# Optimization experiments

Hardware: AMD Instinct MI355X
Metric: run time of the kernel (lower is better)

The kernel has to match this reference:

```python
import jax, jax.numpy as jnp
import numpy as np

D_MODEL = 1024
N_HEADS = 16
HEAD_DIM = D_MODEL // N_HEADS
THETA = 10000.0
NEG = -1e9


def apply_rope(x, positions, theta=THETA):
    # x: (B, H, S, d), positions: (B, 1, S)
    d = x.shape[-1]
    inv_freq = 1.0 / (theta ** (jnp.arange(0, d, 2, dtype=jnp.float32) / d))  # (d/2,)
    freqs = positions[..., None].astype(jnp.float32) * inv_freq  # (B, 1, S, d/2)
    cos, sin = jnp.cos(freqs), jnp.sin(freqs)
    xr = x.reshape(x.shape[:-1] + (d // 2, 2))
    xe, xo = xr[..., 0], xr[..., 1]
    rot = jnp.stack([xe * cos - xo * sin, xe * sin + xo * cos], axis=-1)
    return rot.reshape(x.shape)


def setup_inputs() -> dict:
    key = jax.random.key(0)
    ks = jax.random.split(key, 5)
    B, S = 2, 2048
    scale = 1.0 / np.sqrt(D_MODEL)
    return {
        "x": jax.random.normal(ks[0], (B, S, D_MODEL), dtype=jnp.float32),
        "wq": jax.random.normal(ks[1], (D_MODEL, D_MODEL), dtype=jnp.float32) * scale,
        "wk": jax.random.normal(ks[2], (D_MODEL, D_MODEL), dtype=jnp.float32) * scale,
        "wv": jax.random.normal(ks[3], (D_MODEL, D_MODEL), dtype=jnp.float32) * scale,
        "wo": jax.random.normal(ks[4], (D_MODEL, D_MODEL), dtype=jnp.float32) * scale,
        "token_positions": jnp.arange(S, dtype=jnp.int64),
    }


def reference(x, wq, wk, wv, wo, token_positions):
    B, S, D = x.shape
    H, d = N_HEADS, HEAD_DIM
    # QKV projections (module does x @ w.T)
    q = (x @ wq.T).reshape(B, S, H, d).transpose(0, 2, 1, 3)  # (B, H, S, d)
    k = (x @ wk.T).reshape(B, S, H, d).transpose(0, 2, 1, 3)
    v = (x @ wv.T).reshape(B, S, H, d).transpose(0, 2, 1, 3)
    pos = jnp.broadcast_to(token_positions[None, :], (B, S))[:, None, :]  # (B, 1, S)
    q = apply_rope(q, pos)
    k = apply_rope(k, pos)
    scores = jnp.einsum("bhqd,bhkd->bhqk", q, k) / jnp.sqrt(jnp.float32(d))
    causal = jnp.tril(jnp.ones((S, S), dtype=bool))
    scores = jnp.where(causal[None, None], scores, NEG)
    attn = jax.nn.softmax(scores, axis=-1)
    out = jnp.einsum("bhqk,bhkd->bhqd", attn, v)
    out = out.transpose(0, 2, 1, 3).reshape(B, S, D)
    return out @ wo.T
```

## Files before the change

### kernel.cpp

```cpp
#include <hip/hip_runtime.h>

typedef __bf16 bf16;
typedef __bf16 bf16x8 __attribute__((ext_vector_type(8)));
typedef __bf16 bf16x4 __attribute__((ext_vector_type(4)));
typedef float f32x4 __attribute__((ext_vector_type(4)));
typedef float f32x16 __attribute__((ext_vector_type(16)));
typedef float fx2 __attribute__((ext_vector_type(2)));

#define DEV static __device__ __forceinline__

constexpr int BB = 2, SS = 2048, DM = 1024, NH = 16, HD = 64;
constexpr int MTOT = BB * SS;
constexpr float LOG2E = 1.4426950408889634f;

constexpr size_t OFF_XB   = 0;
constexpr size_t OFF_WQKV = OFF_XB   + (size_t)MTOT * DM * 2;
constexpr size_t OFF_WO   = OFF_WQKV + (size_t)3 * DM * DM * 2;
constexpr size_t OFF_TAB  = OFF_WO   + (size_t)DM * DM * 2;
constexpr size_t OFF_Q    = OFF_TAB  + (size_t)SS * (HD/2) * 8;
constexpr size_t OFF_KF   = OFF_Q    + (size_t)MTOT * DM * 2;
constexpr size_t OFF_VF   = OFF_KF   + (size_t)MTOT * DM * 2;
constexpr size_t OFF_AO   = OFF_VF   + (size_t)MTOT * DM * 2;

typedef const __attribute__((address_space(1))) void gas_void;
typedef __attribute__((address_space(3))) void las_void;

DEV void gload16(const bf16* g, bf16* l) {
  __builtin_amdgcn_global_load_lds((gas_void*)g, (las_void*)l, 16, 0, 0);
}

DEV f32x4 mfma16(bf16x8 a, bf16x8 b, f32x4 c) {
  return __builtin_amdgcn_mfma_f32_16x16x32_bf16(a, b, c, 0, 0, 0);
}

DEV f32x16 mfma32(bf16x8 a, bf16x8 b, f32x16 c) {
  return __builtin_amdgcn_mfma_f32_32x32x16_bf16(a, b, c, 0, 0, 0);
}

DEV unsigned pack2(float a, float b) {
  union { bf16 h[2]; unsigned u; } cv;
  cv.h[0] = (bf16)a; cv.h[1] = (bf16)b;
  return cv.u;
}

__global__ void prep_kernel(const float* __restrict__ x, const float* __restrict__ wq,
    const float* __restrict__ wk, const float* __restrict__ wv, const float* __restrict__ wo,
    const int* __restrict__ pos, bf16* __restrict__ xb, bf16* __restrict__ wqkv,
    bf16* __restrict__ wob, fx2* __restrict__ tab) {
  const int NX4 = MTOT * DM / 4;
  const int NW4 = DM * DM / 4;
  const int TOTC = NX4 + 4 * NW4;
  const int NTAB = SS * (HD / 2);
  const int total = TOTC + NTAB;
  for (int i = blockIdx.x * blockDim.x + threadIdx.x; i < total; i += gridDim.x * blockDim.x) {
    if (i < TOTC) {
      const float* src; bf16* dst; int off;
      if (i < NX4) { src = x; dst = xb; off = i; }
      else {
        int i2 = i - NX4; int which = i2 >> 18; off = i2 & (NW4 - 1);
        src = which == 0 ? wq : which == 1 ? wk : which == 2 ? wv : wo;
        dst = which == 0 ? wqkv : which == 1 ? wqkv + DM * DM : which == 2 ? wqkv + 2 * DM * DM : wob;
      }
      float4 v = ((const float4*)src)[off];
      bf16x4 o4 = { (bf16)v.x, (bf16)v.y, (bf16)v.z, (bf16)v.w };
      ((bf16x4*)dst)[off] = o4;
    } else {
      int e = i - TOTC;
      int s = e >> 5, p = e & 31;
      float invf = __builtin_exp2f(-(float)p * (13.287712379549449f / 32.0f));
      float ang = (float)pos[s] * invf;
      fx2 cs; cs.x = cosf(ang); cs.y = sinf(ang);
      tab[e] = cs;
    }
  }
}

DEV void gemm_bt_128(const bf16* __restrict__ A, const bf16* __restrict__ Bw,
                     int rowA0, int rowB0, f32x4 (&acc)[4][4]) {
  __shared__ __align__(16) bf16 lds[2][2][128 * 32];
  const int t = threadIdx.x, w = t >> 6, lane = t & 63;
  const int wr = w >> 1, wc = w & 1, g = lane >> 4, c = lane & 15;
#pragma unroll
  for (int mi = 0; mi < 4; mi++)
#pragma unroll
    for (int ni = 0; ni < 4; ni++) acc[mi][ni] = (f32x4){0.f, 0.f, 0.f, 0.f};
  const bf16* ga = A + (size_t)(rowA0 + (t >> 2)) * DM + (t & 3) * 8;
  const bf16* gb = Bw + (size_t)(rowB0 + (t >> 2)) * DM + (t & 3) * 8;
  const int arow = wr * 64 + c, brow = wc * 64 + c;
  auto stage = [&](int k0, int buf) {
    bf16* la = &lds[buf][0][0] + w * 512;
    bf16* lb = &lds[buf][1][0] + w * 512;
    gload16(ga + k0,            la);
    gload16(ga + k0 + 64 * DM,  la + 2048);
    gload16(gb + k0,            lb);
    gload16(gb + k0 + 64 * DM,  lb + 2048);
  };
  stage(0, 0);
  __syncthreads();
  int cur = 0;
  for (int k0 = 0; k0 < DM; k0 += 32) {
    if (k0 + 32 < DM) stage(k0 + 32, cur ^ 1);
    const bf16* lA = &lds[cur][0][0];
    const bf16* lB = &lds[cur][1][0];
    bf16x8 af[4], bf_[4];
#pragma unroll
    for (int mi = 0; mi < 4; mi++) af[mi]  = *(const bf16x8*)(lA + (arow + mi * 16) * 32 + g * 8);
#pragma unroll
    for (int ni = 0; ni < 4; ni++) bf_[ni] = *(const bf16x8*)(lB + (brow + ni * 16) * 32 + g * 8);
#pragma unroll
    for (int mi = 0; mi < 4; mi++)
#pragma unroll
      for (int ni = 0; ni < 4; ni++)
        acc[mi][ni] = mfma16(af[mi], bf_[ni], acc[mi][ni]);
    __syncthreads();
    cur ^= 1;
  }
}

__global__ __launch_bounds__(256, 2) void qkv_kernel(const bf16* __restrict__ xb,
    const bf16* __restrict__ wqkv, const fx2* __restrict__ tab,
    bf16* __restrict__ Qb, bf16* __restrict__ KFb, bf16* __restrict__ VFb) {
  f32x4 acc[4][4];
  const int rowA0 = blockIdx.y * 128, rowB0 = blockIdx.x * 128;
  gemm_bt_128(xb, wqkv, rowA0, rowB0, acc);
  const int t = threadIdx.x, w = t >> 6, lane = t & 63;
  const int wr = w >> 1, wc = w & 1, g = lane >> 4, c = lane & 15;
  const int which = rowB0 >> 10;
#pragma unroll
  for (int mi = 0; mi < 4; mi++)
#pragma unroll
    for (int ni = 0; ni < 4; ni++) {
      const int ncol = rowB0 + wc * 64 + ni * 16 + c;
      const int nn = ncol & (DM - 1), h = nn >> 6, dd = nn & 63;
#pragma unroll
      for (int j = 0; j < 4; j++) {
        const int mrow = rowA0 + wr * 64 + mi * 16 + 4 * g + j;
        const int b = mrow >> 11, s = mrow & (SS - 1);
        float v = acc[mi][ni][j];
        if (which < 2) {
          float partner = __shfl_xor(v, 1);
          fx2 cs = tab[s * 32 + (dd >> 1)];
          v = v * cs.x + ((dd & 1) ? partner : -partner) * cs.y;
          if (which == 0) {
            Qb[((size_t)((b * NH + h) * SS + s)) * HD + dd] = (bf16)v;
          } else {
            const int kt = s >> 6, b32 = (s >> 5) & 1, l31 = s & 31;
            const int ds2 = dd >> 4, hi2 = (dd >> 3) & 1, e2 = dd & 7;
            const int lane2 = l31 + 32 * hi2;
            KFb[((((size_t)(b * NH + h) * 32 + kt) * 8) + b32 * 4 + ds2) * 512 + lane2 * 8 + e2] = (bf16)v;
          }
        } else {
          const int t2 = ((rowA0 & (SS - 1)) >> 6) + wr;
          const int e2 = (4 * g + j) & 7;
          const int lane2 = (dd & 31) + 32 * (g >> 1);
          VFb[(((((size_t)(b * NH + h) * 32 + t2) * 2 + (dd >> 5)) * 4 + mi) * 64 + lane2) * 8 + e2] = (bf16)v;
        }
      }
    }
}

__global__ __launch_bounds__(256, 3) void attn_kernel(const bf16* __restrict__ Q,
    const bf16* __restrict__ KF, const bf16* __restrict__ VF, bf16* __restrict__ AO) {
  __shared__ float Om[3][2048];
  __shared__ float Ml[3][32];
  __shared__ float Ll[3][32];
  const int flat = blockIdx.x;
  const int flat2 = (flat & 7) * 128 + (flat >> 3);
  const int bh = flat2 >> 5;
  const int p = flat2 & 31;
  const int w = threadIdx.x >> 6;
  const int lane = threadIdx.x & 63;
  const int q31 = lane & 31, hi = lane >> 5;
  const bf16* Qp = Q + (size_t)bh * SS * HD;
  const bf16* KFp = KF + (size_t)bh * SS * HD;
  const bf16* VFp = VF + (size_t)bh * SS * HD;
  const float SCL = 0.125f * LOG2E;

  auto run_chunk = [&](int qbase, int nt) {
    bf16x8 qb[4];
#pragma unroll
    for (int ds = 0; ds < 4; ds++) {
      bf16x8 xq = *(const bf16x8*)(Qp + (size_t)(qbase + q31) * HD + ds * 16 + hi * 8);
#pragma unroll
      for (int e = 0; e < 8; e++) xq[e] = (bf16)((float)xq[e] * SCL);
      qb[ds] = xq;
    }
    float m_r = -3.0e38f, lsum = 0.f;
    f32x16 o0, o1;
#pragma unroll
    for (int e = 0; e < 16; e++) { o0[e] = 0.f; o1[e] = 0.f; }

    for (int tv = w; tv < nt; tv += 4) {
      const int k0 = tv * 64;
      const bf16* kt = KFp + (size_t)tv * 4096;
      const bf16* vt = VFp + (size_t)tv * 4096;
      f32x16 s0, s1;
#pragma unroll
      for (int e = 0; e < 16; e++) { s0[e] = 0.f; s1[e] = 0.f; }
      {
        bf16x8 kf[4];
#pragma unroll
        for (int ds = 0; ds < 4; ds++)
          kf[ds] = *(const bf16x8*)(kt + (size_t)(ds * 64 + lane) * 8);
#pragma unroll
        for (int ds = 0; ds < 4; ds++) s0 = mfma32(kf[ds], qb[ds], s0);
#pragma unroll
        for (int ds = 0; ds < 4; ds++)
          kf[ds] = *(const bf16x8*)(kt + (size_t)((4 + ds) * 64 + lane) * 8);
#pragma unroll
        for (int ds = 0; ds < 4; ds++) s1 = mfma32(kf[ds], qb[ds], s1);
      }
      if (k0 + 63 > qbase) {
        const int qg = qbase + q31;
#pragma unroll
        for (int r = 0; r < 16; r++) {
          const int kg = k0 + (r & 3) + 8 * (r >> 2) + 4 * hi;
          if (kg > qg)      s0[r] = -1.0e30f;
          if (kg + 32 > qg) s1[r] = -1.0e30f;
        }
      }
      {
        float a[16];
#pragma unroll
        for (int r = 0; r < 16; r++) a[r] = fmaxf(s0[r], s1[r]);
#pragma unroll
        for (int d = 8; d > 0; d >>= 1)
#pragma unroll
          for (int r = 0; r < d; r++) a[r] = fmaxf(a[r], a[r + d]);
        const float pm = fmaxf(a[0], __shfl_xor(a[0], 32));
        if (__any(pm > m_r + 8.0f)) {
          const float mnew = fmaxf(m_r, pm);
          const float alpha = __builtin_exp2f(m_r - mnew);
          lsum *= alpha;
#pragma unroll
          for (int e = 0; e < 16; e++) { o0[e] *= alpha; o1[e] *= alpha; }
          m_r = mnew;
        }
        float b[16];
#pragma unroll
        for (int r = 0; r < 16; r++) {
          s0[r] = __builtin_exp2f(s0[r] - m_r);
          s1[r] = __builtin_exp2f(s1[r] - m_r);
          b[r] = s0[r] + s1[r];
        }
#pragma unroll
        for (int d = 8; d > 0; d >>= 1)
#pragma unroll
          for (int r = 0; r < d; r++) b[r] += b[r + d];
        lsum += b[0] + __shfl_xor(b[0], 32);
      }
      bf16x8 pf[4];
#pragma unroll
      for (int ks = 0; ks < 4; ks++) {
        const int rb = 8 * (ks & 1);
        float va0, va1, va2, va3, vb0, vb1, vb2, vb3;
        if (ks < 2) {
          va0 = s0[rb]; va1 = s0[rb + 1]; va2 = s0[rb + 2]; va3 = s0[rb + 3];
          vb0 = s0[rb + 4]; vb1 = s0[rb + 5]; vb2 = s0[rb + 6]; vb3 = s0[rb + 7];
        } else {
          va0 = s1[rb]; va1 = s1[rb + 1]; va2 = s1[rb + 2]; va3 = s1[rb + 3];
          vb0 = s1[rb + 4]; vb1 = s1[rb + 5]; vb2 = s1[rb + 6]; vb3 = s1[rb + 7];
        }
        const unsigned a01 = pack2(va0, va1), a23 = pack2(va2, va3);
        const unsigned b01 = pack2(vb0, vb1), b23 = pack2(vb2, vb3);
        const unsigned z1 = (unsigned)__shfl_xor((int)(hi ? a01 : b01), 32);
        const unsigned z2 = (unsigned)__shfl_xor((int)(hi ? a23 : b23), 32);
        union { unsigned u[4]; bf16x8 v; } cv;
        cv.u[0] = hi ? z1 : a01;
        cv.u[1] = hi ? z2 : a23;
        cv.u[2] = hi ? b01 : z1;
        cv.u[3] = hi ? b23 : z2;
        pf[ks] = cv.v;
      }
      {
        bf16x8 vf[4];
#pragma unroll
        for (int ks = 0; ks < 4; ks++)
          vf[ks] = *(const bf16x8*)(vt + (size_t)(ks * 64 + lane) * 8);
#pragma unroll
        for (int ks = 0; ks < 4; ks++) o0 = mfma32(vf[ks], pf[ks], o0);
#pragma unroll
        for (int ks = 0; ks < 4; ks++)
          vf[ks] = *(const bf16x8*)(vt + (size_t)((4 + ks) * 64 + lane) * 8);
#pragma unroll
        for (int ks = 0; ks < 4; ks++) o1 = mfma32(vf[ks], pf[ks], o1);
      }
    }
    __syncthreads();
    if (w) {
#pragma unroll
      for (int e = 0; e < 16; e++) {
        const int r = (e & 3) + 8 * (e >> 2) + 4 * hi;
        Om[w - 1][r * 32 + q31] = o0[e];
        Om[w - 1][(r + 32) * 32 + q31] = o1[e];
      }
      if (!hi) { Ml[w - 1][q31] = m_r; Ll[w - 1][q31] = lsum; }
    }
    __syncthreads();
    if (!w) {
      float mi_[3];
#pragma unroll
      for (int i = 0; i < 3; i++) mi_[i] = Ml[i][q31];
      float mm = fmaxf(fmaxf(m_r, mi_[0]), fmaxf(mi_[1], mi_[2]));
      const float aS = __builtin_exp2f(m_r - mm);
      float ai[3];
      float L = aS * lsum;
#pragma unroll
      for (int i = 0; i < 3; i++) {
        ai[i] = __builtin_exp2f(mi_[i] - mm);
        L += ai[i] * Ll[i][q31];
      }
      const float linv = 1.0f / L;
      const int b = bh >> 4, h = bh & 15;
      const size_t rowb = ((size_t)(b * SS + qbase + q31)) * DM + h * HD;
#pragma unroll
      for (int g2 = 0; g2 < 4; g2++) {
        bf16x4 w0v, w1v;
#pragma unroll
        for (int j = 0; j < 4; j++) {
          const int e = 4 * g2 + j;
          const int r = j + 8 * g2 + 4 * hi;
          float v0 = aS * o0[e];
          float v1 = aS * o1[e];
#pragma unroll
          for (int i = 0; i < 3; i++) {
            v0 += ai[i] * Om[i][r * 32 + q31];
            v1 += ai[i] * Om[i][(r + 32) * 32 + q31];
          }
          w0v[j] = (bf16)(v0 * linv);
          w1v[j] = (bf16)(v1 * linv);
        }
        *(bf16x4*)(AO + rowb +      8 * g2 + 4 * hi) = w0v;
        *(bf16x4*)(AO + rowb + 32 + 8 * g2 + 4 * hi) = w1v;
      }
    }
    __syncthreads();
  };

  run_chunk(p * 32, p / 2 + 1);
  const int ph = 63 - p;
  run_chunk(ph * 32, ph / 2 + 1);
}

__global__ __launch_bounds__(256, 2) void oproj_kernel(const bf16* __restrict__ AO,
    const bf16* __restrict__ wob, float* __restrict__ out) {
  f32x4 acc[4][4];
  const int rowA0 = blockIdx.y * 128, rowB0 = blockIdx.x * 128;
  gemm_bt_128(AO, wob, rowA0, rowB0, acc);
  const int t = threadIdx.x, w = t >> 6, lane = t & 63;
  const int wr = w >> 1, wc = w & 1, g = lane >> 4, c = lane & 15;
#pragma unroll
  for (int mi = 0; mi < 4; mi++)
#pragma unroll
    for (int ni = 0; ni < 4; ni++) {
      const int ncol = rowB0 + wc * 64 + ni * 16 + c;
#pragma unroll
      for (int j = 0; j < 4; j++) {
        const int mrow = rowA0 + wr * 64 + mi * 16 + 4 * g + j;
        out[(size_t)mrow * DM + ncol] = acc[mi][ni][j];
      }
    }
}

extern "C" void kernel_launch(void* const* d_in, const int* in_sizes, int n_in,
                              void* d_out, int out_size, void* d_ws, size_t ws_size,
                              hipStream_t stream) {
  const float* x  = (const float*)d_in[0];
  const float* wq = (const float*)d_in[1];
  const float* wk = (const float*)d_in[2];
  const float* wv = (const float*)d_in[3];
  const float* wo = (const float*)d_in[4];
  const int*   pos = (const int*)d_in[5];
  char* ws = (char*)d_ws;
  bf16* xb   = (bf16*)(ws + OFF_XB);
  bf16* wqkv = (bf16*)(ws + OFF_WQKV);
  bf16* wob  = (bf16*)(ws + OFF_WO);
  fx2*  tab  = (fx2*)(ws + OFF_TAB);
  bf16* Qb   = (bf16*)(ws + OFF_Q);
  bf16* KFb  = (bf16*)(ws + OFF_KF);
  bf16* VFb  = (bf16*)(ws + OFF_VF);
  bf16* AOb  = (bf16*)(ws + OFF_AO);

  hipLaunchKernelGGL(prep_kernel, dim3(2048), dim3(256), 0, stream,
                     x, wq, wk, wv, wo, pos, xb, wqkv, wob, tab);
  hipLaunchKernelGGL(qkv_kernel, dim3(24, 32), dim3(256), 0, stream,
                     xb, wqkv, tab, Qb, KFb, VFb);
  hipLaunchKernelGGL(attn_kernel, dim3(1024), dim3(256), 0, stream,
                     Qb, KFb, VFb, AOb);
  hipLaunchKernelGGL(oproj_kernel, dim3(8, 32), dim3(256), 0, stream,
                     AOb, wob, (float*)d_out);
}
```

Measured before the change: 123.6 us.

## Stage QKV epilogue through LDS for coalesced 16-byte global stores

The QKV GEMM epilogue now writes RoPE-rotated Q/K and V values into a shared-memory tile laid out in the final Q, KF and VF formats, then copies the tile out with contiguous bf16x8 stores instead of scattered 2-byte stores. The GEMM's LDS buffer is passed in so the same 32 KB can be reused for this staging. qkv_kernel launch bounds are raised to 3 blocks per SM, which may increase register pressure. The change adds an extra barrier and an LDS round trip in exchange for coalesced writes.

New measurement: 119.5 us. 1.03x faster.

```diff
diff --git a/kernel.cpp b/kernel.cpp
--- a/kernel.cpp
+++ b/kernel.cpp
@@ -76,8 +76,7 @@
 }
 
 DEV void gemm_bt_128(const bf16* __restrict__ A, const bf16* __restrict__ Bw,
-                     int rowA0, int rowB0, f32x4 (&acc)[4][4]) {
-  __shared__ __align__(16) bf16 lds[2][2][128 * 32];
+                     int rowA0, int rowB0, f32x4 (&acc)[4][4], bf16* lds) {
   const int t = threadIdx.x, w = t >> 6, lane = t & 63;
   const int wr = w >> 1, wc = w & 1, g = lane >> 4, c = lane & 15;
 #pragma unroll
@@ -88,8 +87,8 @@
   const bf16* gb = Bw + (size_t)(rowB0 + (t >> 2)) * DM + (t & 3) * 8;
   const int arow = wr * 64 + c, brow = wc * 64 + c;
   auto stage = [&](int k0, int buf) {
-    bf16* la = &lds[buf][0][0] + w * 512;
-    bf16* lb = &lds[buf][1][0] + w * 512;
+    bf16* la = lds + buf * 8192 + w * 512;
+    bf16* lb = lds + buf * 8192 + 4096 + w * 512;
     gload16(ga + k0,            la);
     gload16(ga + k0 + 64 * DM,  la + 2048);
     gload16(gb + k0,            lb);
@@ -100,8 +99,8 @@
   int cur = 0;
   for (int k0 = 0; k0 < DM; k0 += 32) {
     if (k0 + 32 < DM) stage(k0 + 32, cur ^ 1);
-    const bf16* lA = &lds[cur][0][0];
-    const bf16* lB = &lds[cur][1][0];
+    const bf16* lA = lds + cur * 8192;
+    const bf16* lB = lds + cur * 8192 + 4096;
     bf16x8 af[4], bf_[4];
 #pragma unroll
     for (int mi = 0; mi < 4; mi++) af[mi]  = *(const bf16x8*)(lA + (arow + mi * 16) * 32 + g * 8);
@@ -117,46 +116,72 @@
   }
 }
 
-__global__ __launch_bounds__(256, 2) void qkv_kernel(const bf16* __restrict__ xb,
+__global__ __launch_bounds__(256, 3) void qkv_kernel(const bf16* __restrict__ xb,
     const bf16* __restrict__ wqkv, const fx2* __restrict__ tab,
     bf16* __restrict__ Qb, bf16* __restrict__ KFb, bf16* __restrict__ VFb) {
+  __shared__ __align__(16) bf16 L[16384];
   f32x4 acc[4][4];
   const int rowA0 = blockIdx.y * 128, rowB0 = blockIdx.x * 128;
-  gemm_bt_128(xb, wqkv, rowA0, rowB0, acc);
+  gemm_bt_128(xb, wqkv, rowA0, rowB0, acc, L);
   const int t = threadIdx.x, w = t >> 6, lane = t & 63;
   const int wr = w >> 1, wc = w & 1, g = lane >> 4, c = lane & 15;
   const int which = rowB0 >> 10;
+  const int b = rowA0 >> 11;
+  const int s0 = rowA0 & (SS - 1);
+  const int h0 = (rowB0 & (DM - 1)) >> 6;
+  const int kt0 = s0 >> 6;
 #pragma unroll
   for (int mi = 0; mi < 4; mi++)
 #pragma unroll
     for (int ni = 0; ni < 4; ni++) {
-      const int ncol = rowB0 + wc * 64 + ni * 16 + c;
-      const int nn = ncol & (DM - 1), h = nn >> 6, dd = nn & 63;
+      const int col = wc * 64 + ni * 16 + c;
+      const int hh = col >> 6, dd = col & 63;
 #pragma unroll
       for (int j = 0; j < 4; j++) {
-        const int mrow = rowA0 + wr * 64 + mi * 16 + 4 * g + j;
-        const int b = mrow >> 11, s = mrow & (SS - 1);
+        const int sp = wr * 64 + mi * 16 + 4 * g + j;
         float v = acc[mi][ni][j];
+        int flat;
         if (which < 2) {
+          const int s = s0 + sp;
           float partner = __shfl_xor(v, 1);
           fx2 cs = tab[s * 32 + (dd >> 1)];
           v = v * cs.x + ((dd & 1) ? partner : -partner) * cs.y;
           if (which == 0) {
-            Qb[((size_t)((b * NH + h) * SS + s)) * HD + dd] = (bf16)v;
+            flat = hh * 8192 + sp * 64 + dd;
           } else {
-            const int kt = s >> 6, b32 = (s >> 5) & 1, l31 = s & 31;
-            const int ds2 = dd >> 4, hi2 = (dd >> 3) & 1, e2 = dd & 7;
-            const int lane2 = l31 + 32 * hi2;
-            KFb[((((size_t)(b * NH + h) * 32 + kt) * 8) + b32 * 4 + ds2) * 512 + lane2 * 8 + e2] = (bf16)v;
+            const int spp = sp & 63;
+            flat = (hh * 2 + (sp >> 6)) * 4096 +
+                   (((spp >> 5) * 4 + (dd >> 4)) * 64 + (spp & 31) + 32 * ((dd >> 3) & 1)) * 8 +
+                   (dd & 7);
           }
         } else {
-          const int t2 = ((rowA0 & (SS - 1)) >> 6) + wr;
-          const int e2 = (4 * g + j) & 7;
-          const int lane2 = (dd & 31) + 32 * (g >> 1);
-          VFb[(((((size_t)(b * NH + h) * 32 + t2) * 2 + (dd >> 5)) * 4 + mi) * 64 + lane2) * 8 + e2] = (bf16)v;
-        }
-      }
-    }
+          const int spp = sp & 63;
+          flat = (hh * 2 + (sp >> 6)) * 4096 +
+                 (((dd >> 5) * 4 + mi) * 64 + (dd & 31) + 32 * (g >> 1)) * 8 + (spp & 7);
+        }
+        L[flat] = (bf16)v;
+      }
+    }
+  __syncthreads();
+  if (which == 0) {
+    bf16* base0 = Qb + ((size_t)(b * NH + h0) * SS + s0) * HD;
+    bf16* base1 = Qb + ((size_t)(b * NH + h0 + 1) * SS + s0) * HD;
+#pragma unroll
+    for (int j2 = 0; j2 < 8; j2++) {
+      const int off = j2 * 2048 + t * 8;
+      bf16* dst = (off < 8192 ? base0 : base1) + (off & 8191);
+      *(bf16x8*)dst = *(const bf16x8*)(L + off);
+    }
+  } else {
+    bf16* outp = (which == 1) ? KFb : VFb;
+#pragma unroll
+    for (int j2 = 0; j2 < 8; j2++) {
+      const int off = j2 * 2048 + t * 8;
+      const int r = off >> 12;
+      bf16* dst = outp + ((size_t)(b * NH + h0 + (r >> 1)) * 32 + kt0 + (r & 1)) * 4096 + (off & 4095);
+      *(bf16x8*)dst = *(const bf16x8*)(L + off);
+    }
+  }
 }
 
 __global__ __launch_bounds__(256, 3) void attn_kernel(const bf16* __restrict__ Q,
@@ -304,13 +329,13 @@
       float mm = fmaxf(fmaxf(m_r, mi_[0]), fmaxf(mi_[1], mi_[2]));
       const float aS = __builtin_exp2f(m_r - mm);
       float ai[3];
-      float L = aS * lsum;
+      float L2 = aS * lsum;
 #pragma unroll
       for (int i = 0; i < 3; i++) {
         ai[i] = __builtin_exp2f(mi_[i] - mm);
-        L += ai[i] * Ll[i][q31];
-      }
-      const float linv = 1.0f / L;
+        L2 += ai[i] * Ll[i][q31];
+      }
+      const float linv = 1.0f / L2;
       const int b = bh >> 4, h = bh & 15;
       const size_t rowb = ((size_t)(b * SS + qbase + q31)) * DM + h * HD;
 #pragma unroll
@@ -344,9 +369,10 @@
 
 __global__ __launch_bounds__(256, 2) void oproj_kernel(const bf16* __restrict__ AO,
     const bf16* __restrict__ wob, float* __restrict__ out) {
+  __shared__ __align__(16) bf16 L[16384];
   f32x4 acc[4][4];
   const int rowA0 = blockIdx.y * 128, rowB0 = blockIdx.x * 128;
-  gemm_bt_128(AO, wob, rowA0, rowB0, acc);
+  gemm_bt_128(AO, wob, rowA0, rowB0, acc, L);
   const int t = threadIdx.x, w = t >> 6, lane = t & 63;
   const int wr = w >> 1, wc = w & 1, g = lane >> 4, c = lane & 15;
 #pragma unroll
```
